# Kernel optimization log

Hardware: AMD Instinct MI355X
Metric: run time of the kernel (lower is better)

Reference implementation:

```python
import jax, jax.numpy as jnp
import numpy as np

NEG_SLOPE = 0.2
EPS = 1e-16

N_NODES = 50000
N_EDGES = 1600000
IN_CH = 256
HID = 16
HEADS = 2


def setup_inputs() -> dict:
    key = jax.random.key(0)
    ks = jax.random.split(key, 12)
    s = lambda k, shape, scale=0.1: jax.random.normal(k, shape, dtype=jnp.float32) * scale
    x = jax.random.normal(ks[0], (N_NODES, IN_CH), dtype=jnp.float32)
    edge_index = jax.random.randint(ks[1], (2, N_EDGES), 0, N_NODES, dtype=jnp.int64)
    return {
        "x": x,
        "edge_index": edge_index,
        "W1": s(ks[2], (IN_CH, HEADS * HID)),
        "att_src1": s(ks[3], (HEADS, HID)),
        "att_dst1": s(ks[4], (HEADS, HID)),
        "b1": jnp.zeros((HEADS * HID,), jnp.float32),
        "W2": s(ks[5], (HEADS * HID, HID)),
        "att_src2": s(ks[6], (1, HID)),
        "att_dst2": s(ks[7], (1, HID)),
        "b2": jnp.zeros((HID,), jnp.float32),
        "Wm1": s(ks[8], (2 * HID, HID)),
        "bm1": jnp.zeros((HID,), jnp.float32),
        "Wm2": s(ks[9], (HID, 1)),
        "bm2": jnp.zeros((1,), jnp.float32),
    }


def gat_conv(x, src, dst, W, att_src, att_dst, bias, heads, out_ch, concat):
    # x: [N, F] -> h: [N, H, C]
    n = x.shape[0]
    h = (x @ W).reshape(n, heads, out_ch)
    # per-node attention logits [N, H]
    a_src = jnp.sum(h * att_src, axis=-1)
    a_dst = jnp.sum(h * att_dst, axis=-1)
    # per-edge logits: message j (src) -> i (dst); softmax grouped by dst
    e = a_src[src] + a_dst[dst]                      # [E, H]
    e = jax.nn.leaky_relu(e, NEG_SLOPE)
    e_max = jax.ops.segment_max(e, dst, num_segments=n)
    e_exp = jnp.exp(e - e_max[dst])
    denom = jax.ops.segment_sum(e_exp, dst, num_segments=n)
    alpha = e_exp / (denom[dst] + EPS)               # [E, H]
    msg = alpha[:, :, None] * h[src]                 # [E, H, C]
    out = jax.ops.segment_sum(msg, dst, num_segments=n)  # [N, H, C]
    out = out.reshape(n, heads * out_ch) if concat else out.mean(axis=1)
    return out + bias


def reference(x, edge_index, W1, att_src1, att_dst1, b1,
              W2, att_src2, att_dst2, b2, Wm1, bm1, Wm2, bm2):
    src, dst = edge_index[0], edge_index[1]
    # eval mode: feature/attention dropout are identity
    h = gat_conv(x, src, dst, W1, att_src1, att_dst1, b1, HEADS, HID, concat=True)
    h = jax.nn.elu(h)
    h = gat_conv(h, src, dst, W2, att_src2, att_dst2, b2, 1, HID, concat=False)
    # edge MLP on gathered (src, dst) node pairs
    ef = jnp.concatenate([h[src], h[dst]], axis=-1)  # [E, 2*HID]
    ef = jax.nn.relu(ef @ Wm1 + bm1)
    flow = (ef @ Wm2 + bm2).squeeze(-1)              # [E]
    return jax.nn.relu(flow)
```

## Files before the change

kernel.cpp:

```cpp
#include <hip/hip_runtime.h>
#include <hip/hip_bf16.h>
#include <hip/hip_fp16.h>

#define N_NODES 50000
#define N_EDGES 1600000
#define IN_CH 256
#define NEG_SLOPE 0.2f
#define EPS_F 1e-16f
#define CNT_PAD 16
#define CAP 128
#define NBK 196
#define CAPB 10240
#define PCHUNK 3125
#define KTILE 64
#define XS_PITCH (KTILE + 4)

__device__ __forceinline__ float lrelu(float x) {
    return x > 0.f ? x : NEG_SLOPE * x;
}

__device__ __forceinline__ float2 h2f(unsigned int w) {
    __half2 h;
    *reinterpret_cast<unsigned int*>(&h) = w;
    return __half22float2(h);
}

__device__ __forceinline__ unsigned int f2h2(float a, float b) {
    __half2 h = __floats2half2_rn(a, b);
    return *reinterpret_cast<unsigned int*>(&h);
}

__global__ __launch_bounds__(256) void k0_detect(const int* __restrict__ ei,
                                                 int* __restrict__ flag,
                                                 int* __restrict__ gcnt)
{
    __shared__ int nz;
    const int t = threadIdx.x;
    if (t == 0) nz = 0;
    if (t < 256) gcnt[t] = 0;
    __syncthreads();
    if (t & 1) { if (ei[t] != 0) atomicAdd(&nz, 1); }
    __syncthreads();
    if (t == 0) flag[0] = (nz == 0) ? 1 : 0;
}

__device__ __forceinline__ int ld_src(const int* ei, int f, int e) {
    return f ? ei[2 * (size_t)e] : ei[e];
}
__device__ __forceinline__ int ld_dst(const int* ei, int f, int e) {
    return f ? ei[2 * (size_t)N_EDGES + 2 * (size_t)e]
             : ei[(size_t)N_EDGES + e];
}

__global__ __launch_bounds__(1024) void k_part(const int* __restrict__ ei,
                                               const int* __restrict__ flag,
                                               int* __restrict__ gcnt,
                                               int2* __restrict__ bseg)
{
    __shared__ int hist[NBK];
    __shared__ int cur[NBK];
    const int t = threadIdx.x;
    for (int j = t; j < NBK; j += 1024) hist[j] = 0;
    __syncthreads();
    const int f = flag[0];
    const int e0 = blockIdx.x * PCHUNK;
    const int e1 = min(e0 + PCHUNK, N_EDGES);
    for (int e = e0 + t; e < e1; e += 1024)
        atomicAdd(&hist[ld_dst(ei, f, e) >> 8], 1);
    __syncthreads();
    for (int j = t; j < NBK; j += 1024)
        cur[j] = j * CAPB + atomicAdd(&gcnt[j], hist[j]);
    __syncthreads();
    for (int e = e0 + t; e < e1; e += 1024) {
        const int s = ld_src(ei, f, e);
        const int d = ld_dst(ei, f, e);
        const int bk = d >> 8;
        const int pos = atomicAdd(&cur[bk], 1);
        if (pos - bk * CAPB < CAPB) bseg[pos] = make_int2(s, d);
    }
}

__global__ __launch_bounds__(1024) void k_sub(const int* __restrict__ gcnt,
                                              const int2* __restrict__ bseg,
                                              int* __restrict__ cnt,
                                              int* __restrict__ csr_src)
{
    __shared__ int cur[256];
    const int b = blockIdx.x;
    const int t = threadIdx.x;
    if (t < 256) cur[t] = 0;
    __syncthreads();
    const int count = min(gcnt[b], CAPB);
    const int2* seg = bseg + (size_t)b * CAPB;
    for (int i = t; i < count; i += 1024) {
        const int2 e = seg[i];
        const int slot = atomicAdd(&cur[e.y & 255], 1);
        if (slot < CAP) csr_src[((size_t)e.y << 7) + slot] = e.x;
    }
    __syncthreads();
    if (t < 256) {
        const int n = b * 256 + t;
        if (n < N_NODES) cnt[(size_t)n * CNT_PAD] = min(cur[t], CAP);
    }
}

__global__ __launch_bounds__(256) void k1_gemm1(
    const float* __restrict__ x, const float* __restrict__ W1,
    const float* __restrict__ att_src1, const float* __restrict__ att_dst1,
    __half* __restrict__ h1, float* __restrict__ a_src1, float* __restrict__ a_dst1)
{
    __shared__ float w1s[IN_CH * 32];
    __shared__ float xs[64 * XS_PITCH];
    __shared__ float attss[32], attds[32];
    const int t = threadIdx.x;
    for (int i = t; i < IN_CH * 32; i += 256) w1s[i] = W1[i];
    if (t < 32) { attss[t] = att_src1[t]; attds[t] = att_dst1[t]; }
    const int row0 = blockIdx.x * 64;
    const int colq = t & 7, c4 = colq * 4;
    const int rp = t >> 3;
    const int r0 = rp * 2, r1 = r0 + 1;
    float4 a0 = make_float4(0.f, 0.f, 0.f, 0.f);
    float4 a1 = make_float4(0.f, 0.f, 0.f, 0.f);
    for (int kb = 0; kb < IN_CH; kb += KTILE) {
        __syncthreads();
        #pragma unroll
        for (int i = 0; i < 4; ++i) {
            const int idx = t + 256 * i;
            const int r = idx >> 4, p = idx & 15;
            const int row = row0 + r;
            float4 vv = make_float4(0.f, 0.f, 0.f, 0.f);
            if (row < N_NODES)
                vv = *(const float4*)(x + (size_t)row * IN_CH + kb + p * 4);
            *(float4*)(&xs[r * XS_PITCH + p * 4]) = vv;
        }
        __syncthreads();
        #pragma unroll 8
        for (int kt = 0; kt < KTILE; ++kt) {
            const float xv0 = xs[r0 * XS_PITCH + kt];
            const float xv1 = xs[r1 * XS_PITCH + kt];
            const float4 wv = *(const float4*)(&w1s[(kb + kt) * 32 + c4]);
            a0.x += xv0 * wv.x; a0.y += xv0 * wv.y;
            a0.z += xv0 * wv.z; a0.w += xv0 * wv.w;
            a1.x += xv1 * wv.x; a1.y += xv1 * wv.y;
            a1.z += xv1 * wv.z; a1.w += xv1 * wv.w;
        }
    }
    const int row_a = row0 + r0, row_b = row0 + r1;
    if (row_a < N_NODES) {
        uint2 p; p.x = f2h2(a0.x, a0.y); p.y = f2h2(a0.z, a0.w);
        *(uint2*)(h1 + (size_t)row_a * 32 + c4) = p;
    }
    if (row_b < N_NODES) {
        uint2 p; p.x = f2h2(a1.x, a1.y); p.y = f2h2(a1.z, a1.w);
        *(uint2*)(h1 + (size_t)row_b * 32 + c4) = p;
    }
    float sa0 = a0.x * attss[c4] + a0.y * attss[c4 + 1]
              + a0.z * attss[c4 + 2] + a0.w * attss[c4 + 3];
    float sd0 = a0.x * attds[c4] + a0.y * attds[c4 + 1]
              + a0.z * attds[c4 + 2] + a0.w * attds[c4 + 3];
    float sa1 = a1.x * attss[c4] + a1.y * attss[c4 + 1]
              + a1.z * attss[c4 + 2] + a1.w * attss[c4 + 3];
    float sd1 = a1.x * attds[c4] + a1.y * attds[c4 + 1]
              + a1.z * attds[c4 + 2] + a1.w * attds[c4 + 3];
    sa0 += __shfl_xor(sa0, 1); sa0 += __shfl_xor(sa0, 2);
    sd0 += __shfl_xor(sd0, 1); sd0 += __shfl_xor(sd0, 2);
    sa1 += __shfl_xor(sa1, 1); sa1 += __shfl_xor(sa1, 2);
    sd1 += __shfl_xor(sd1, 1); sd1 += __shfl_xor(sd1, 2);
    const int head = colq >> 2;
    if ((colq & 3) == 0) {
        if (row_a < N_NODES) {
            a_src1[row_a * 2 + head] = sa0;
            a_dst1[row_a * 2 + head] = sd0;
        }
        if (row_b < N_NODES) {
            a_src1[row_b * 2 + head] = sa1;
            a_dst1[row_b * 2 + head] = sd1;
        }
    }
}

__global__ __launch_bounds__(256) void k_agg1(
    const int* __restrict__ cnt, const int* __restrict__ csr_src,
    const float* __restrict__ a_src1, const float* __restrict__ a_dst1,
    const __half* __restrict__ h1, float* __restrict__ out1)
{
    const int wid = (blockIdx.x * 256 + threadIdx.x) >> 6;
    const int lane = threadIdx.x & 63;
    if (wid >= N_NODES) return;
    const int len = min(cnt[(size_t)wid * CNT_PAD], CAP);
    const int beg = wid << 7, end = beg + len;
    const float2 ad = *(const float2*)(a_dst1 + 2 * (size_t)wid);
    const int slot = lane >> 4, chp = lane & 15;
    const int head = chp >> 3;
    const float adh = head ? ad.y : ad.x;
    const int rep = ((chp & 7) == 0);
    const unsigned int* __restrict__ h1u = (const unsigned int*)h1;
    float accx = 0.f, accy = 0.f, sw = 0.f;
    int i = beg + slot;
    for (; i + 28 < end; i += 32) {
        int s[8]; float a[8]; unsigned int hw[8]; float w[8];
        #pragma unroll
        for (int j = 0; j < 8; ++j) s[j] = csr_src[i + 4 * j];
        #pragma unroll
        for (int j = 0; j < 8; ++j) a[j] = a_src1[2 * (size_t)s[j] + head];
        #pragma unroll
        for (int j = 0; j < 8; ++j) hw[j] = h1u[(size_t)s[j] * 16 + chp];
        #pragma unroll
        for (int j = 0; j < 8; ++j) w[j] = __expf(lrelu(a[j] + adh));
        float wsum = 0.f;
        #pragma unroll
        for (int j = 0; j < 8; ++j) {
            const float2 hf = h2f(hw[j]);
            wsum += w[j];
            accx += w[j] * hf.x; accy += w[j] * hf.y;
        }
        if (rep) sw += wsum;
    }
    for (; i + 12 < end; i += 16) {
        int s[4]; float a[4]; unsigned int hw[4]; float w[4];
        #pragma unroll
        for (int j = 0; j < 4; ++j) s[j] = csr_src[i + 4 * j];
        #pragma unroll
        for (int j = 0; j < 4; ++j) a[j] = a_src1[2 * (size_t)s[j] + head];
        #pragma unroll
        for (int j = 0; j < 4; ++j) hw[j] = h1u[(size_t)s[j] * 16 + chp];
        #pragma unroll
        for (int j = 0; j < 4; ++j) w[j] = __expf(lrelu(a[j] + adh));
        float wsum = 0.f;
        #pragma unroll
        for (int j = 0; j < 4; ++j) {
            const float2 hf = h2f(hw[j]);
            wsum += w[j];
            accx += w[j] * hf.x; accy += w[j] * hf.y;
        }
        if (rep) sw += wsum;
    }
    for (; i < end; i += 4) {
        const int s = csr_src[i];
        const float w = __expf(lrelu(a_src1[2 * (size_t)s + head] + adh));
        if (rep) sw += w;
        const float2 hf = h2f(h1u[(size_t)s * 16 + chp]);
        accx += w * hf.x; accy += w * hf.y;
    }
    sw += __shfl_xor(sw, 16); sw += __shfl_xor(sw, 32);
    const float swh = __shfl(sw, head << 3);
    accx += __shfl_xor(accx, 16); accx += __shfl_xor(accx, 32);
    accy += __shfl_xor(accy, 16); accy += __shfl_xor(accy, 32);
    const float inv = 1.f / (swh + EPS_F);
    if (lane < 16) {
        float2 o; o.x = accx * inv; o.y = accy * inv;
        *(float2*)(out1 + (size_t)wid * 32 + 2 * chp) = o;
    }
}

__global__ __launch_bounds__(256) void k4_layer2(
    const float* __restrict__ out1, const float* __restrict__ b1,
    const float* __restrict__ W2, const float* __restrict__ att_src2,
    const float* __restrict__ att_dst2,
    __half* __restrict__ h2, float* __restrict__ a_src2, float* __restrict__ a_dst2)
{
    __shared__ float act[16][32];
    __shared__ float w2s[32 * 16];
    __shared__ float b1s[32], as2[16], ad2[16];
    const int t = threadIdx.x;
    for (int i = t; i < 512; i += 256) w2s[i] = W2[i];
    if (t < 32) b1s[t] = b1[t];
    if (t < 16) { as2[t] = att_src2[t]; ad2[t] = att_dst2[t]; }
    __syncthreads();
    const int node0 = blockIdx.x * 16;
    for (int i = t; i < 512; i += 256) {
        const int nl = i >> 5, k = i & 31;
        const int row = node0 + nl;
        float v = 0.f;
        if (row < N_NODES) {
            v = out1[(size_t)row * 32 + k] + b1s[k];
            v = v > 0.f ? v : expm1f(v);
        }
        act[nl][k] = v;
    }
    __syncthreads();
    const int nl = t >> 4, j = t & 15;
    const int row = node0 + nl;
    float acc = 0.f;
    #pragma unroll
    for (int k = 0; k < 32; ++k) acc += act[nl][k] * w2s[k * 16 + j];
    if (row < N_NODES) h2[(size_t)row * 16 + j] = __float2half(acc);
    float sa = acc * as2[j], sd = acc * ad2[j];
    #pragma unroll
    for (int m = 1; m < 16; m <<= 1) { sa += __shfl_xor(sa, m); sd += __shfl_xor(sd, m); }
    if (j == 0 && row < N_NODES) { a_src2[row] = sa; a_dst2[row] = sd; }
}

__global__ __launch_bounds__(256) void k_agg2(
    const int* __restrict__ cnt, const int* __restrict__ csr_src,
    const float* __restrict__ a_src2, const float* __restrict__ a_dst2,
    const __half* __restrict__ h2, float* __restrict__ out2)
{
    const int wid = (blockIdx.x * 256 + threadIdx.x) >> 6;
    const int lane = threadIdx.x & 63;
    if (wid >= N_NODES) return;
    const int len = min(cnt[(size_t)wid * CNT_PAD], CAP);
    const int beg = wid << 7, end = beg + len;
    const float ad = a_dst2[wid];
    const int slot = lane >> 3, chp = lane & 7;
    const int rep = (chp == 0);
    const unsigned int* __restrict__ h2u = (const unsigned int*)h2;
    float accx = 0.f, accy = 0.f, sw = 0.f;
    int i = beg + slot;
    for (; i + 24 < end; i += 32) {
        int s[4]; float a[4]; unsigned int hw[4]; float w[4];
        #pragma unroll
        for (int j = 0; j < 4; ++j) s[j] = csr_src[i + 8 * j];
        #pragma unroll
        for (int j = 0; j < 4; ++j) a[j] = a_src2[s[j]];
        #pragma unroll
        for (int j = 0; j < 4; ++j) hw[j] = h2u[(size_t)s[j] * 8 + chp];
        #pragma unroll
        for (int j = 0; j < 4; ++j) w[j] = __expf(lrelu(a[j] + ad));
        float wsum = 0.f;
        #pragma unroll
        for (int j = 0; j < 4; ++j) {
            const float2 hf = h2f(hw[j]);
            wsum += w[j];
            accx += w[j] * hf.x; accy += w[j] * hf.y;
        }
        if (rep) sw += wsum;
    }
    for (; i < end; i += 8) {
        const int s = csr_src[i];
        const float w = __expf(lrelu(a_src2[s] + ad));
        if (rep) sw += w;
        const float2 hf = h2f(h2u[(size_t)s * 8 + chp]);
        accx += w * hf.x; accy += w * hf.y;
    }
    sw += __shfl_xor(sw, 8); sw += __shfl_xor(sw, 16); sw += __shfl_xor(sw, 32);
    const float swt = __shfl(sw, 0);
    accx += __shfl_xor(accx, 8); accx += __shfl_xor(accx, 16); accx += __shfl_xor(accx, 32);
    accy += __shfl_xor(accy, 8); accy += __shfl_xor(accy, 16); accy += __shfl_xor(accy, 32);
    const float inv = 1.f / (swt + EPS_F);
    if (lane < 8) {
        float2 o; o.x = accx * inv; o.y = accy * inv;
        *(float2*)(out2 + (size_t)wid * 16 + 2 * chp) = o;
    }
}

__global__ __launch_bounds__(256) void k_prep(
    const float* __restrict__ out2, const float* __restrict__ b2,
    const float* __restrict__ Wm1, const float* __restrict__ bm1,
    __half* __restrict__ u, __half* __restrict__ v)
{
    __shared__ float wa[16 * 16], wb[16 * 16];
    __shared__ float act[16][17];
    __shared__ float b2s[16], bm1s[16];
    const int t = threadIdx.x;
    if (t < 256) {
        const int k = t >> 4, j = t & 15;
        wa[t] = Wm1[k * 16 + j];
        wb[t] = Wm1[(16 + k) * 16 + j];
    }
    if (t < 16) { b2s[t] = b2[t]; bm1s[t] = bm1[t]; }
    __syncthreads();
    const int node0 = blockIdx.x * 16;
    const int nl = t >> 4, c = t & 15;
    const int row = node0 + nl;
    act[nl][c] = (row < N_NODES) ? out2[(size_t)row * 16 + c] + b2s[c] : 0.f;
    __syncthreads();
    float su = bm1s[c], sv = 0.f;
    #pragma unroll
    for (int k = 0; k < 16; ++k) {
        const float a = act[nl][k];
        su += a * wa[k * 16 + c];
        sv += a * wb[k * 16 + c];
    }
    if (row < N_NODES) {
        u[(size_t)row * 16 + c] = __float2half(su);
        v[(size_t)row * 16 + c] = __float2half(sv);
    }
}

__global__ __launch_bounds__(256) void k7_lite(
    const int* __restrict__ ei, const int* __restrict__ flag,
    const __half* __restrict__ u, const __half* __restrict__ v,
    const float* __restrict__ Wm2, const float* __restrict__ bm2,
    float* __restrict__ out)
{
    __shared__ float wm2s[16];
    __shared__ float bm2s;
    const int t = threadIdx.x;
    if (t < 16) wm2s[t] = Wm2[t];
    if (t == 0) bm2s = bm2[0];
    __syncthreads();
    const int e = blockIdx.x * 256 + t;
    if (e >= N_EDGES) return;
    const int f = flag[0];
    const int s = ld_src(ei, f, e);
    const int d = ld_dst(ei, f, e);
    const uint4* up = (const uint4*)(u + (size_t)s * 16);
    const uint4* vp = (const uint4*)(v + (size_t)d * 16);
    const uint4 ua = up[0], ub = up[1];
    const uint4 va = vp[0], vb = vp[1];
    float fl = bm2s;
    unsigned int uw[8] = {ua.x, ua.y, ua.z, ua.w, ub.x, ub.y, ub.z, ub.w};
    unsigned int vw[8] = {va.x, va.y, va.z, va.w, vb.x, vb.y, vb.z, vb.w};
    #pragma unroll
    for (int i = 0; i < 8; ++i) {
        const float2 a = h2f(uw[i]);
        const float2 b = h2f(vw[i]);
        fl += fmaxf(a.x + b.x, 0.f) * wm2s[2 * i];
        fl += fmaxf(a.y + b.y, 0.f) * wm2s[2 * i + 1];
    }
    out[e] = fmaxf(fl, 0.f);
}

extern "C" void kernel_launch(void* const* d_in, const int* in_sizes, int n_in,
                              void* d_out, int out_size, void* d_ws, size_t ws_size,
                              hipStream_t stream)
{
    const float* x        = (const float*)d_in[0];
    const int*   ei       = (const int*)d_in[1];
    const float* W1       = (const float*)d_in[2];
    const float* att_src1 = (const float*)d_in[3];
    const float* att_dst1 = (const float*)d_in[4];
    const float* b1       = (const float*)d_in[5];
    const float* W2       = (const float*)d_in[6];
    const float* att_src2 = (const float*)d_in[7];
    const float* att_dst2 = (const float*)d_in[8];
    const float* b2       = (const float*)d_in[9];
    const float* Wm1      = (const float*)d_in[10];
    const float* bm1      = (const float*)d_in[11];
    const float* Wm2      = (const float*)d_in[12];
    const float* bm2      = (const float*)d_in[13];

    float* ws = (float*)d_ws;
    size_t off = 0;
    __half* h1 = (__half*)(ws + off); off += 16 * (size_t)N_NODES;
    float* a_src1 = ws + off; off += 2  * (size_t)N_NODES;
    float* a_dst1 = ws + off; off += 2  * (size_t)N_NODES;
    float* out1   = ws + off; off += 32 * (size_t)N_NODES;
    __half* h2 = (__half*)(ws + off); off += 16 * (size_t)N_NODES;
    float* a_src2 = ws + off; off += 1  * (size_t)N_NODES;
    float* a_dst2 = ws + off; off += 1  * (size_t)N_NODES;
    float* out2   = ws + off; off += 16 * (size_t)N_NODES;
    __half* u = (__half*)(ws + off); off += 8 * (size_t)N_NODES;
    __half* v = (__half*)(ws + off); off += 8 * (size_t)N_NODES;
    int* cnt     = (int*)(ws + off); off += (size_t)N_NODES * CNT_PAD;
    int* csr_src = (int*)(ws + off); off += (size_t)N_NODES * CAP;
    int* gcnt    = (int*)(ws + off); off += 256;
    int* flag    = (int*)(ws + off); off += 64;
    int2* bseg = (int2*)ws;

    k0_detect<<<1, 256, 0, stream>>>(ei, flag, gcnt);
    k_part<<<(N_EDGES + PCHUNK - 1) / PCHUNK, 1024, 0, stream>>>(ei, flag, gcnt, bseg);
    k_sub<<<NBK, 1024, 0, stream>>>(gcnt, bseg, cnt, csr_src);

    k1_gemm1<<<(N_NODES + 63) / 64, 256, 0, stream>>>(
        x, W1, att_src1, att_dst1, h1, a_src1, a_dst1);
    k_agg1<<<(N_NODES + 3) / 4, 256, 0, stream>>>(
        cnt, csr_src, a_src1, a_dst1, h1, out1);
    k4_layer2<<<(N_NODES + 15) / 16, 256, 0, stream>>>(
        out1, b1, W2, att_src2, att_dst2, h2, a_src2, a_dst2);
    k_agg2<<<(N_NODES + 3) / 4, 256, 0, stream>>>(
        cnt, csr_src, a_src2, a_dst2, h2, out2);
    k_prep<<<(N_NODES + 15) / 16, 256, 0, stream>>>(
        out2, b2, Wm1, bm1, u, v);
    k7_lite<<<(N_EDGES + 255) / 256, 256, 0, stream>>>(
        ei, flag, u, v, Wm2, bm2, (float*)d_out);
}
```

Measured before the change: 259.7 us.

## Fuse per-node layer-2 and edge-MLP prep into aggregation kernels, inline dtype detect

Folds the dense per-node transforms (bias+ELU+W2 projection with attention logits, and bias+Wm1 projection into u/v) into the epilogues of the two aggregation kernels. This drops two launches and the global round-trips of out1 and out2. The int64 detection kernel is replaced by a per-wave ballot inside k_part and k7_lite, plus a memset for gcnt. In exchange the aggregation kernels carry extra shared memory and a block barrier, and every wave re-reads the first 128 index words.

```diff
diff --git a/kernel.cpp b/kernel.cpp
--- a/kernel.cpp
+++ b/kernel.cpp
@@ -30,18 +30,10 @@
     return *reinterpret_cast<unsigned int*>(&h);
 }
 
-__global__ __launch_bounds__(256) void k0_detect(const int* __restrict__ ei,
-                                                 int* __restrict__ flag,
-                                                 int* __restrict__ gcnt)
-{
-    __shared__ int nz;
-    const int t = threadIdx.x;
-    if (t == 0) nz = 0;
-    if (t < 256) gcnt[t] = 0;
-    __syncthreads();
-    if (t & 1) { if (ei[t] != 0) atomicAdd(&nz, 1); }
-    __syncthreads();
-    if (t == 0) flag[0] = (nz == 0) ? 1 : 0;
+__device__ __forceinline__ int detect_i64(const int* __restrict__ ei) {
+    const int lane = threadIdx.x & 63;
+    const unsigned long long b = __ballot(ei[2 * lane + 1] != 0);
+    return b == 0ull ? 1 : 0;
 }
 
 __device__ __forceinline__ int ld_src(const int* ei, int f, int e) {
@@ -53,16 +45,15 @@
 }
 
 __global__ __launch_bounds__(1024) void k_part(const int* __restrict__ ei,
-                                               const int* __restrict__ flag,
                                                int* __restrict__ gcnt,
                                                int2* __restrict__ bseg)
 {
     __shared__ int hist[NBK];
     __shared__ int cur[NBK];
     const int t = threadIdx.x;
+    const int f = detect_i64(ei);
     for (int j = t; j < NBK; j += 1024) hist[j] = 0;
     __syncthreads();
-    const int f = flag[0];
     const int e0 = blockIdx.x * PCHUNK;
     const int e1 = min(e0 + PCHUNK, N_EDGES);
     for (int e = e0 + t; e < e1; e += 1024)
@@ -179,17 +170,30 @@
     }
 }
 
-__global__ __launch_bounds__(256) void k_agg1(
+__global__ __launch_bounds__(256) void k_agg1f(
     const int* __restrict__ cnt, const int* __restrict__ csr_src,
     const float* __restrict__ a_src1, const float* __restrict__ a_dst1,
-    const __half* __restrict__ h1, float* __restrict__ out1)
-{
-    const int wid = (blockIdx.x * 256 + threadIdx.x) >> 6;
-    const int lane = threadIdx.x & 63;
-    if (wid >= N_NODES) return;
-    const int len = min(cnt[(size_t)wid * CNT_PAD], CAP);
+    const __half* __restrict__ h1,
+    const float* __restrict__ b1, const float* __restrict__ W2,
+    const float* __restrict__ att_src2, const float* __restrict__ att_dst2,
+    __half* __restrict__ h2, float* __restrict__ a_src2, float* __restrict__ a_dst2)
+{
+    __shared__ float w2s[32 * 16];
+    __shared__ float b1s[32], as2[16], ad2[16];
+    __shared__ float act_s[4][32];
+    const int t = threadIdx.x;
+    for (int i = t; i < 512; i += 256) w2s[i] = W2[i];
+    if (t < 32) b1s[t] = b1[t];
+    if (t < 16) { as2[t] = att_src2[t]; ad2[t] = att_dst2[t]; }
+
+    const int wid = (blockIdx.x * 256 + t) >> 6;
+    const int lane = t & 63;
+    const int wv = t >> 6;
+    const int active = (wid < N_NODES);
+    const int len = active ? min(cnt[(size_t)wid * CNT_PAD], CAP) : 0;
     const int beg = wid << 7, end = beg + len;
-    const float2 ad = *(const float2*)(a_dst1 + 2 * (size_t)wid);
+    float2 ad = make_float2(0.f, 0.f);
+    if (active) ad = *(const float2*)(a_dst1 + 2 * (size_t)wid);
     const int slot = lane >> 4, chp = lane & 15;
     const int head = chp >> 3;
     const float adh = head ? ad.y : ad.x;
@@ -248,60 +252,49 @@
     accy += __shfl_xor(accy, 16); accy += __shfl_xor(accy, 32);
     const float inv = 1.f / (swh + EPS_F);
     if (lane < 16) {
-        float2 o; o.x = accx * inv; o.y = accy * inv;
-        *(float2*)(out1 + (size_t)wid * 32 + 2 * chp) = o;
-    }
-}
-
-__global__ __launch_bounds__(256) void k4_layer2(
-    const float* __restrict__ out1, const float* __restrict__ b1,
-    const float* __restrict__ W2, const float* __restrict__ att_src2,
-    const float* __restrict__ att_dst2,
-    __half* __restrict__ h2, float* __restrict__ a_src2, float* __restrict__ a_dst2)
-{
-    __shared__ float act[16][32];
-    __shared__ float w2s[32 * 16];
-    __shared__ float b1s[32], as2[16], ad2[16];
-    const int t = threadIdx.x;
-    for (int i = t; i < 512; i += 256) w2s[i] = W2[i];
-    if (t < 32) b1s[t] = b1[t];
-    if (t < 16) { as2[t] = att_src2[t]; ad2[t] = att_dst2[t]; }
-    __syncthreads();
-    const int node0 = blockIdx.x * 16;
-    for (int i = t; i < 512; i += 256) {
-        const int nl = i >> 5, k = i & 31;
-        const int row = node0 + nl;
-        float v = 0.f;
-        if (row < N_NODES) {
-            v = out1[(size_t)row * 32 + k] + b1s[k];
-            v = v > 0.f ? v : expm1f(v);
-        }
-        act[nl][k] = v;
-    }
-    __syncthreads();
-    const int nl = t >> 4, j = t & 15;
-    const int row = node0 + nl;
-    float acc = 0.f;
+        float ax = accx * inv + b1s[2 * chp];
+        float ay = accy * inv + b1s[2 * chp + 1];
+        ax = ax > 0.f ? ax : expm1f(ax);
+        ay = ay > 0.f ? ay : expm1f(ay);
+        act_s[wv][2 * chp] = ax;
+        act_s[wv][2 * chp + 1] = ay;
+    }
+    __syncthreads();
+    const int j = lane & 15;
+    float acc2 = 0.f;
     #pragma unroll
-    for (int k = 0; k < 32; ++k) acc += act[nl][k] * w2s[k * 16 + j];
-    if (row < N_NODES) h2[(size_t)row * 16 + j] = __float2half(acc);
-    float sa = acc * as2[j], sd = acc * ad2[j];
-    #pragma unroll
-    for (int m = 1; m < 16; m <<= 1) { sa += __shfl_xor(sa, m); sd += __shfl_xor(sd, m); }
-    if (j == 0 && row < N_NODES) { a_src2[row] = sa; a_dst2[row] = sd; }
-}
-
-__global__ __launch_bounds__(256) void k_agg2(
+    for (int k = 0; k < 32; ++k) acc2 += act_s[wv][k] * w2s[k * 16 + j];
+    if (lane < 16 && active) h2[(size_t)wid * 16 + j] = __float2half(acc2);
+    float sa = acc2 * as2[j], sd = acc2 * ad2[j];
+    sa += __shfl_xor(sa, 1); sa += __shfl_xor(sa, 2);
+    sa += __shfl_xor(sa, 4); sa += __shfl_xor(sa, 8);
+    sd += __shfl_xor(sd, 1); sd += __shfl_xor(sd, 2);
+    sd += __shfl_xor(sd, 4); sd += __shfl_xor(sd, 8);
+    if (lane == 0 && active) { a_src2[wid] = sa; a_dst2[wid] = sd; }
+}
+
+__global__ __launch_bounds__(256) void k_agg2f(
     const int* __restrict__ cnt, const int* __restrict__ csr_src,
     const float* __restrict__ a_src2, const float* __restrict__ a_dst2,
-    const __half* __restrict__ h2, float* __restrict__ out2)
-{
-    const int wid = (blockIdx.x * 256 + threadIdx.x) >> 6;
-    const int lane = threadIdx.x & 63;
-    if (wid >= N_NODES) return;
-    const int len = min(cnt[(size_t)wid * CNT_PAD], CAP);
+    const __half* __restrict__ h2,
+    const float* __restrict__ b2, const float* __restrict__ Wm1,
+    const float* __restrict__ bm1,
+    __half* __restrict__ u, __half* __restrict__ v)
+{
+    __shared__ float wa[16 * 16], wb[16 * 16];
+    __shared__ float b2s[16], bm1s[16];
+    __shared__ float act_s[4][16];
+    const int t = threadIdx.x;
+    if (t < 256) { wa[t] = Wm1[t]; wb[t] = Wm1[256 + t]; }
+    if (t < 16) { b2s[t] = b2[t]; bm1s[t] = bm1[t]; }
+
+    const int wid = (blockIdx.x * 256 + t) >> 6;
+    const int lane = t & 63;
+    const int wv = t >> 6;
+    const int active = (wid < N_NODES);
+    const int len = active ? min(cnt[(size_t)wid * CNT_PAD], CAP) : 0;
     const int beg = wid << 7, end = beg + len;
-    const float ad = a_dst2[wid];
+    const float ad = active ? a_dst2[wid] : 0.f;
     const int slot = lane >> 3, chp = lane & 7;
     const int rep = (chp == 0);
     const unsigned int* __restrict__ h2u = (const unsigned int*)h2;
@@ -339,47 +332,28 @@
     accy += __shfl_xor(accy, 8); accy += __shfl_xor(accy, 16); accy += __shfl_xor(accy, 32);
     const float inv = 1.f / (swt + EPS_F);
     if (lane < 8) {
-        float2 o; o.x = accx * inv; o.y = accy * inv;
-        *(float2*)(out2 + (size_t)wid * 16 + 2 * chp) = o;
-    }
-}
-
-__global__ __launch_bounds__(256) void k_prep(
-    const float* __restrict__ out2, const float* __restrict__ b2,
-    const float* __restrict__ Wm1, const float* __restrict__ bm1,
-    __half* __restrict__ u, __half* __restrict__ v)
-{
-    __shared__ float wa[16 * 16], wb[16 * 16];
-    __shared__ float act[16][17];
-    __shared__ float b2s[16], bm1s[16];
-    const int t = threadIdx.x;
-    if (t < 256) {
-        const int k = t >> 4, j = t & 15;
-        wa[t] = Wm1[k * 16 + j];
-        wb[t] = Wm1[(16 + k) * 16 + j];
-    }
-    if (t < 16) { b2s[t] = b2[t]; bm1s[t] = bm1[t]; }
-    __syncthreads();
-    const int node0 = blockIdx.x * 16;
-    const int nl = t >> 4, c = t & 15;
-    const int row = node0 + nl;
-    act[nl][c] = (row < N_NODES) ? out2[(size_t)row * 16 + c] + b2s[c] : 0.f;
-    __syncthreads();
+        float2 o;
+        o.x = accx * inv + b2s[2 * chp];
+        o.y = accy * inv + b2s[2 * chp + 1];
+        *(float2*)(&act_s[wv][2 * chp]) = o;
+    }
+    __syncthreads();
+    const int c = lane & 15;
     float su = bm1s[c], sv = 0.f;
     #pragma unroll
     for (int k = 0; k < 16; ++k) {
-        const float a = act[nl][k];
+        const float a = act_s[wv][k];
         su += a * wa[k * 16 + c];
         sv += a * wb[k * 16 + c];
     }
-    if (row < N_NODES) {
-        u[(size_t)row * 16 + c] = __float2half(su);
-        v[(size_t)row * 16 + c] = __float2half(sv);
+    if (lane < 16 && active) {
+        u[(size_t)wid * 16 + c] = __float2half(su);
+        v[(size_t)wid * 16 + c] = __float2half(sv);
     }
 }
 
 __global__ __launch_bounds__(256) void k7_lite(
-    const int* __restrict__ ei, const int* __restrict__ flag,
+    const int* __restrict__ ei,
     const __half* __restrict__ u, const __half* __restrict__ v,
     const float* __restrict__ Wm2, const float* __restrict__ bm2,
     float* __restrict__ out)
@@ -387,12 +361,12 @@
     __shared__ float wm2s[16];
     __shared__ float bm2s;
     const int t = threadIdx.x;
+    const int f = detect_i64(ei);
     if (t < 16) wm2s[t] = Wm2[t];
     if (t == 0) bm2s = bm2[0];
     __syncthreads();
     const int e = blockIdx.x * 256 + t;
     if (e >= N_EDGES) return;
-    const int f = flag[0];
     const int s = ld_src(ei, f, e);
     const int d = ld_dst(ei, f, e);
     const uint4* up = (const uint4*)(u + (size_t)s * 16);
@@ -436,33 +410,31 @@
     __half* h1 = (__half*)(ws + off); off += 16 * (size_t)N_NODES;
     float* a_src1 = ws + off; off += 2  * (size_t)N_NODES;
     float* a_dst1 = ws + off; off += 2  * (size_t)N_NODES;
-    float* out1   = ws + off; off += 32 * (size_t)N_NODES;
+    float* out1_dead = ws + off; off += 32 * (size_t)N_NODES;
     __half* h2 = (__half*)(ws + off); off += 16 * (size_t)N_NODES;
     float* a_src2 = ws + off; off += 1  * (size_t)N_NODES;
     float* a_dst2 = ws + off; off += 1  * (size_t)N_NODES;
-    float* out2   = ws + off; off += 16 * (size_t)N_NODES;
+    float* out2_dead = ws + off; off += 16 * (size_t)N_NODES;
     __half* u = (__half*)(ws + off); off += 8 * (size_t)N_NODES;
     __half* v = (__half*)(ws + off); off += 8 * (size_t)N_NODES;
     int* cnt     = (int*)(ws + off); off += (size_t)N_NODES * CNT_PAD;
     int* csr_src = (int*)(ws + off); off += (size_t)N_NODES * CAP;
     int* gcnt    = (int*)(ws + off); off += 256;
     int* flag    = (int*)(ws + off); off += 64;
+    (void)out1_dead; (void)out2_dead; (void)flag;
     int2* bseg = (int2*)ws;
 
-    k0_detect<<<1, 256, 0, stream>>>(ei, flag, gcnt);
-    k_part<<<(N_EDGES + PCHUNK - 1) / PCHUNK, 1024, 0, stream>>>(ei, flag, gcnt, bseg);
+    hipMemsetAsync(gcnt, 0, 256 * sizeof(int), stream);
+    k_part<<<(N_EDGES + PCHUNK - 1) / PCHUNK, 1024, 0, stream>>>(ei, gcnt, bseg);
     k_sub<<<NBK, 1024, 0, stream>>>(gcnt, bseg, cnt, csr_src);
 
     k1_gemm1<<<(N_NODES + 63) / 64, 256, 0, stream>>>(
         x, W1, att_src1, att_dst1, h1, a_src1, a_dst1);
-    k_agg1<<<(N_NODES + 3) / 4, 256, 0, stream>>>(
-        cnt, csr_src, a_src1, a_dst1, h1, out1);
-    k4_layer2<<<(N_NODES + 15) / 16, 256, 0, stream>>>(
-        out1, b1, W2, att_src2, att_dst2, h2, a_src2, a_dst2);
-    k_agg2<<<(N_NODES + 3) / 4, 256, 0, stream>>>(
-        cnt, csr_src, a_src2, a_dst2, h2, out2);
-    k_prep<<<(N_NODES + 15) / 16, 256, 0, stream>>>(
-        out2, b2, Wm1, bm1, u, v);
+    k_agg1f<<<(N_NODES + 3) / 4, 256, 0, stream>>>(
+        cnt, csr_src, a_src1, a_dst1, h1, b1, W2, att_src2, att_dst2,
+        h2, a_src2, a_dst2);
+    k_agg2f<<<(N_NODES + 3) / 4, 256, 0, stream>>>(
+        cnt, csr_src, a_src2, a_dst2, h2, b2, Wm1, bm1, u, v);
     k7_lite<<<(N_EDGES + 255) / 256, 256, 0, stream>>>(
-        ei, flag, u, v, Wm2, bm2, (float*)d_out);
-}
+        ei, u, v, Wm2, bm2, (float*)d_out);
+}
```

Result: no change. 259.3 us (-0.2%).
